# Kernel optimization log

Measured on AMD Instinct MI355X. Metric: run time of the kernel, lower is better.

## Reference

```python
import jax, jax.numpy as jnp
import numpy as np

B, S, D = 4, 2048, 1024
H = 16
HS = D // H  # 64


def setup_inputs() -> dict:
    key = jax.random.key(0)
    ks = jax.random.split(key, 6)
    scale = 1.0 / np.sqrt(D)
    x = jax.random.normal(ks[0], (B, S, D), dtype=jnp.float32)
    # per-head projection weights, stacked: [H, D, HS]
    Wq = jax.random.normal(ks[1], (H, D, HS), dtype=jnp.float32) * scale
    Wk = jax.random.normal(ks[2], (H, D, HS), dtype=jnp.float32) * scale
    Wv = jax.random.normal(ks[3], (H, D, HS), dtype=jnp.float32) * scale
    Wo = jax.random.normal(ks[4], (D, D), dtype=jnp.float32) * scale
    bo = jax.random.normal(ks[5], (D,), dtype=jnp.float32) * 0.01
    return {"x": x, "Wq": Wq, "Wk": Wk, "Wv": Wv, "Wo": Wo, "bo": bo}


def reference(x, Wq, Wk, Wv, Wo, bo):
    # Per-head dense projections (no bias): [B,S,D] x [H,D,HS] -> [B,H,S,HS]
    q = jnp.einsum('bsd,hde->bhse', x, Wq)
    k = jnp.einsum('bsd,hde->bhse', x, Wk)
    v = jnp.einsum('bsd,hde->bhse', x, Wv)
    # scaled dot-product scores: [B,H,S,S]
    scores = jnp.einsum('bhse,bhte->bhst', q, k) / jnp.sqrt(jnp.asarray(HS, dtype=x.dtype))
    # causal mask (lower triangular kept)
    causal = jnp.tril(jnp.ones((S, S), dtype=bool))
    scores = jnp.where(causal, scores, -jnp.inf)
    attn = jax.nn.softmax(scores, axis=-1)
    # dropout is identity at inference (rate handled as 0)
    out = jnp.einsum('bhst,bhte->bhse', attn, v)  # [B,H,S,HS]
    # concat heads: [B,S,H*HS] = [B,S,D]
    out = jnp.transpose(out, (0, 2, 1, 3)).reshape(B, S, D)
    return out @ Wo + bo
```

## Files before the change

kernel.cpp:

```cpp
#include <hip/hip_runtime.h>
#include <hip/hip_bf16.h>
#include <stdint.h>

#define NB 4
#define NS 2048
#define ND 1024
#define NH 16
#define NHS 64
#define NEG_BIG (-1e30f)
#define Q_SCALE 0.18033688011112042f

typedef __bf16 bf16x8 __attribute__((ext_vector_type(8)));
typedef float floatx4 __attribute__((ext_vector_type(4)));
typedef short s16x4 __attribute__((ext_vector_type(4)));

#if defined(__has_builtin)
#if __has_builtin(__builtin_amdgcn_mfma_f32_16x16x16bf16_1k)
#define HAVE_MFMA1K 1
#endif
#endif
#ifndef HAVE_MFMA1K
#define HAVE_MFMA1K 0
#endif

static constexpr size_t WSLAB = (size_t)NH * ND * NHS;
static constexpr size_t QSLAB = (size_t)NB * NH * NS * NHS;
static constexpr size_t XSLAB = (size_t)NB * NS * ND;

__device__ __forceinline__ uint16_t f2b(float f) {
    union { __hip_bfloat16 h; uint16_t u; } cv;
    cv.h = __float2bfloat16(f);
    return cv.u;
}

__device__ __forceinline__ void gll16(const void* g, void* l) {
  __builtin_amdgcn_global_load_lds(
      (__attribute__((address_space(1))) void*)(uintptr_t)g,
      (__attribute__((address_space(3))) void*)(uintptr_t)l,
      16, 0, 0);
}

__global__ __launch_bounds__(256) void k_prep(
    const float* __restrict__ x, const float* __restrict__ Wq,
    const float* __restrict__ Wk, const float* __restrict__ Wv,
    const float* __restrict__ Wo, uint16_t* __restrict__ xb,
    uint16_t* __restrict__ wt) {
  __shared__ __align__(16) uint16_t T[64][72];
  int bid = blockIdx.x;
  int tid = threadIdx.x;
  if (bid < 4096) {
    size_t i0 = ((size_t)bid * 256 + tid) * 8;
    float4 f0 = *(const float4*)&x[i0];
    float4 f1 = *(const float4*)&x[i0 + 4];
    __align__(16) uint16_t tmp[8];
    tmp[0] = f2b(f0.x); tmp[1] = f2b(f0.y); tmp[2] = f2b(f0.z); tmp[3] = f2b(f0.w);
    tmp[4] = f2b(f1.x); tmp[5] = f2b(f1.y); tmp[6] = f2b(f1.z); tmp[7] = f2b(f1.w);
    *(uint4*)&xb[i0] = *(uint4*)tmp;
    return;
  }
  bid -= 4096;
  const float* src; uint16_t* dst;
  int srcStride, dstStride, r0, c0;
  if (bid < 768) {
    int mat = bid >> 8;
    int rem = bid & 255;
    int h = rem >> 4, dt = rem & 15;
    const float* W = (mat == 0) ? Wq : (mat == 1) ? Wk : Wv;
    src = W + (size_t)h * (ND * NHS);
    dst = wt + (size_t)mat * WSLAB + (size_t)h * (NHS * ND);
    srcStride = NHS; dstStride = ND;
    r0 = dt * 64; c0 = 0;
  } else {
    int rem = bid - 768;
    int dt = rem >> 4, et = rem & 15;
    src = Wo; dst = wt + 3 * WSLAB;
    srcStride = ND; dstStride = ND;
    r0 = dt * 64; c0 = et * 64;
  }
  for (int u = tid; u < 1024; u += 256) {
    int row = u >> 4, cq = u & 15;
    float4 f = *(const float4*)&src[(size_t)(r0 + row) * srcStride + c0 + cq * 4];
    uint16_t* p = &T[row][cq * 4];
    p[0] = f2b(f.x); p[1] = f2b(f.y); p[2] = f2b(f.z); p[3] = f2b(f.w);
  }
  __syncthreads();
  for (int u = tid; u < 512; u += 256) {
    int c = u >> 3, cg = u & 7;
    __align__(16) uint16_t tmp[8];
    for (int j = 0; j < 8; j++) tmp[j] = T[cg * 8 + j][c];
    *(uint4*)&dst[(size_t)(c0 + c) * dstStride + r0 + cg * 8] = *(uint4*)tmp;
  }
}

__global__ __launch_bounds__(512, 4) void k_qkv(
    const uint16_t* __restrict__ xb, const uint16_t* __restrict__ wt,
    uint16_t* __restrict__ qk, uint16_t* __restrict__ vt) {
  __shared__ __align__(16) uint16_t L[32768];

  int bid = blockIdx.x;
  int xcd = bid & 7, idx = bid >> 3;
  int mtile = xcd * 8 + (idx & 7);
  int ntile = idx >> 3;
  int m0 = mtile * 128;
  int n0 = ntile * 128;

  int tid = threadIdx.x;
  int wave = tid >> 6, lane = tid & 63, quad = lane >> 4, l16 = lane & 15;
  int wr = wave >> 2, wc = wave & 3;

  int swc = ((tid & 3) ^ ((tid >> 4) & 3)) * 8;
  const uint16_t* pA = xb + (size_t)(m0 + (tid >> 2)) * ND + swc;
  const uint16_t* pB = wt + (size_t)(n0 + (tid >> 2)) * ND + swc;
  const int stOff = wave * 512;

  const int rq = (quad ^ (l16 >> 2)) * 8;
  const int offA = (wr * 64 + l16) * 32 + rq;
  const int offB = (wc * 32 + l16) * 32 + rq;

  floatx4 acc[4][2];
  #pragma unroll
  for (int i = 0; i < 4; i++)
    #pragma unroll
    for (int j = 0; j < 2; j++) acc[i][j] = (floatx4){0.f, 0.f, 0.f, 0.f};

#define STAGE(A_)                                                               \
  do {                                                                          \
    int a_ = (A_);                                                              \
    if (a_ < 32) {                                                              \
      int ko_ = (a_ >> 1) * 64 + (a_ & 1) * 32;                                 \
      gll16(pA + ko_, &L[(a_ & 3) * 4096 + stOff]);                             \
      gll16(pB + ko_, &L[16384 + (a_ & 3) * 4096 + stOff]);                     \
    }                                                                           \
  } while (0)

#define PH_BAR()                         \
  do {                                   \
    asm volatile("" ::: "memory");       \
    __builtin_amdgcn_s_barrier();        \
    asm volatile("" ::: "memory");       \
  } while (0)

  STAGE(0); STAGE(1); STAGE(2);
  asm volatile("s_waitcnt vmcnt(4)" ::: "memory");
  PH_BAR();

#define MFMA8()                                                                           \
  _Pragma("unroll")                                                                       \
  for (int mt_ = 0; mt_ < 4; mt_++)                                                       \
    _Pragma("unroll")                                                                     \
    for (int nt_ = 0; nt_ < 2; nt_++)                                                     \
      acc[mt_][nt_] = __builtin_amdgcn_mfma_f32_16x16x32_bf16(af[mt_], bfr[nt_], acc[mt_][nt_], 0, 0, 0)

  for (int t = 0; t < 16; ++t) {
    {
      int sA = ((2 * t) & 3) * 4096;
      int sB = 16384 + ((2 * t) & 3) * 4096;
      bf16x8 af[4], bfr[2];
      #pragma unroll
      for (int i = 0; i < 4; i++) af[i] = *(const bf16x8*)&L[sA + offA + i * 512];
      #pragma unroll
      for (int i = 0; i < 2; i++) bfr[i] = *(const bf16x8*)&L[sB + offB + i * 512];
      STAGE(2 * t + 3);
      PH_BAR();
      __builtin_amdgcn_s_setprio(1);
      MFMA8();
      __builtin_amdgcn_s_setprio(0);
      if (t < 15) { asm volatile("s_waitcnt vmcnt(4)" ::: "memory"); }
      else        { asm volatile("s_waitcnt vmcnt(0)" ::: "memory"); }
      PH_BAR();
    }
    {
      int sA = ((2 * t + 1) & 3) * 4096;
      int sB = 16384 + ((2 * t + 1) & 3) * 4096;
      bf16x8 af[4], bfr[2];
      #pragma unroll
      for (int i = 0; i < 4; i++) af[i] = *(const bf16x8*)&L[sA + offA + i * 512];
      #pragma unroll
      for (int i = 0; i < 2; i++) bfr[i] = *(const bf16x8*)&L[sB + offB + i * 512];
      STAGE(2 * t + 4);
      PH_BAR();
      __builtin_amdgcn_s_setprio(1);
      MFMA8();
      __builtin_amdgcn_s_setprio(0);
      if (t < 14)       { asm volatile("s_waitcnt vmcnt(4)" ::: "memory"); }
      else if (t == 14) { asm volatile("s_waitcnt vmcnt(2)" ::: "memory"); }
      if (t < 15) PH_BAR();
    }
  }
#undef MFMA8
#undef STAGE
#undef PH_BAR

  int matid = n0 >> 10;
  int b = m0 >> 11;
  if (matid == 2) {
    int hh = ((n0 - 2048) >> 6) + (wc >> 1);
    #pragma unroll
    for (int nt = 0; nt < 2; nt++) {
      int e = (wc & 1) * 32 + nt * 16 + l16;
      uint16_t* vrow = vt + ((size_t)(b * 16 + hh) * 64 + e) * NS;
      #pragma unroll
      for (int mt = 0; mt < 4; mt++) {
        __align__(8) uint16_t t4v[4];
        #pragma unroll
        for (int r = 0; r < 4; r++) t4v[r] = f2b(acc[mt][nt][r]);
        int s = (m0 & 2047) + wr * 64 + mt * 16 + quad * 4;
        *(uint2*)&vrow[s] = *(uint2*)t4v;
      }
    }
  } else {
    float scale = (matid == 0) ? Q_SCALE : 1.0f;
    uint16_t* base = qk + (size_t)matid * QSLAB;
    int hh = ((n0 & 1023) >> 6) + (wc >> 1);
    #pragma unroll
    for (int mt = 0; mt < 4; mt++) {
      int s = (m0 & 2047) + wr * 64 + mt * 16 + quad * 4;
      size_t rbase = ((size_t)(b * 16 + hh) * NS + s) * NHS;
      #pragma unroll
      for (int nt = 0; nt < 2; nt++)
        #pragma unroll
        for (int r = 0; r < 4; r++)
          base[rbase + (size_t)r * NHS + (wc & 1) * 32 + nt * 16 + l16] =
              f2b(acc[mt][nt][r] * scale);
    }
  }
}

#if HAVE_MFMA1K
__global__ __launch_bounds__(256, 4) void k_attn(
    const uint16_t* __restrict__ Q, const uint16_t* __restrict__ K,
    const uint16_t* __restrict__ VT, uint16_t* __restrict__ Y) {
  __shared__ __align__(16) uint16_t Ks[2][4096];
  __shared__ __align__(16) uint16_t Vs[2][4096];
  int bid = blockIdx.x;
  int bh = bid & 63;
  int w = bid >> 6;
  int ta = (w & 8) ? (15 - (w & 7)) : w;
  int b = bh >> 4, h = bh & 15;
  int tb = 31 - ta;
  const uint16_t* Qp = Q + (size_t)bh * (NS * NHS);
  const uint16_t* Kp = K + (size_t)bh * (NS * NHS);
  const uint16_t* Vp = VT + (size_t)bh * (NS * NHS);
  int tid = threadIdx.x;
  int wv = tid >> 6, lane = tid & 63, quad = lane >> 4, l16 = lane & 15;

  int srow = lane >> 3;
  int swOff = ((lane & 7) ^ srow) * 8;
  int stRow0 = wv * 16 + srow;
  int stRow1 = wv * 16 + 8 + srow;
  const int dst0 = wv * 1024;
  const int dst1 = wv * 1024 + 512;

#define STAGE_KV(KT, BUF)                                                         \
  do {                                                                            \
    int kt_ = (KT);                                                               \
    gll16(Kp + (size_t)(kt_ * 64 + stRow0) * NHS + swOff, &Ks[BUF][dst0]);        \
    gll16(Kp + (size_t)(kt_ * 64 + stRow1) * NHS + swOff, &Ks[BUF][dst1]);        \
    gll16(Vp + (size_t)stRow0 * NS + kt_ * 64 + swOff, &Vs[BUF][dst0]);           \
    gll16(Vp + (size_t)stRow1 * NS + kt_ * 64 + swOff, &Vs[BUF][dst1]);           \
  } while (0)

  int e3 = l16 & 7;
  int kc0 = (quad ^ e3) * 8;
  int kc1 = ((4 | quad) ^ e3) * 8;
  int vql = (quad & 1) * 4;
  int vqh = quad >> 1;
  int vcol[4];
  #pragma unroll
  for (int ct = 0; ct < 4; ct++)
    vcol[ct] = (((ct * 2 + vqh) ^ e3) * 8) + vql;

  int rA = ta * 64 + wv * 16 + l16;
  int rB = tb * 64 + wv * 16 + l16;
  bf16x8 aqA0 = *(const bf16x8*)&Qp[(size_t)rA * NHS + quad * 8];
  bf16x8 aqA1 = *(const bf16x8*)&Qp[(size_t)rA * NHS + 32 + quad * 8];
  bf16x8 aqB0 = *(const bf16x8*)&Qp[(size_t)rB * NHS + quad * 8];
  bf16x8 aqB1 = *(const bf16x8*)&Qp[(size_t)rB * NHS + 32 + quad * 8];

  float lAs = 0.f, lBs = 0.f;
  floatx4 oA[4], oB[4];
  for (int et = 0; et < 4; et++) {
    oA[et] = (floatx4){0.f, 0.f, 0.f, 0.f};
    oB[et] = (floatx4){0.f, 0.f, 0.f, 0.f};
  }

  STAGE_KV(0, 0);
  __syncthreads();

  for (int kt = 0; kt <= tb; kt++) {
    int cur = kt & 1;
    if (kt < tb) STAGE_KV(kt + 1, cur ^ 1);
    const uint16_t* KB = &Ks[cur][0];
    const uint16_t* VB = &Vs[cur][0];
    bool doA = (kt <= ta);

    s16x4 pbA[4], pbB[4];
    #pragma unroll
    for (int ct = 0; ct < 4; ct++) {
      int krow = (ct * 16 + l16) * 64;
      bf16x8 kb0 = *(const bf16x8*)&KB[krow + kc0];
      bf16x8 kb1 = *(const bf16x8*)&KB[krow + kc1];
      int key = kt * 64 + ct * 16 + quad * 4;
      floatx4 c = (floatx4){0.f, 0.f, 0.f, 0.f};
      c = __builtin_amdgcn_mfma_f32_16x16x32_bf16(kb0, aqB0, c, 0, 0, 0);
      c = __builtin_amdgcn_mfma_f32_16x16x32_bf16(kb1, aqB1, c, 0, 0, 0);
      #pragma unroll
      for (int r = 0; r < 4; r++) {
        float s = (kt == tb && key + r > rB) ? NEG_BIG : c[r];
        float p = __builtin_amdgcn_exp2f(s);
        lBs += p;
        pbB[ct][r] = (short)f2b(p);
      }
      if (doA) {
        floatx4 d = (floatx4){0.f, 0.f, 0.f, 0.f};
        d = __builtin_amdgcn_mfma_f32_16x16x32_bf16(kb0, aqA0, d, 0, 0, 0);
        d = __builtin_amdgcn_mfma_f32_16x16x32_bf16(kb1, aqA1, d, 0, 0, 0);
        #pragma unroll
        for (int r = 0; r < 4; r++) {
          float s = (kt == ta && key + r > rA) ? NEG_BIG : d[r];
          float p = __builtin_amdgcn_exp2f(s);
          lAs += p;
          pbA[ct][r] = (short)f2b(p);
        }
      }
    }
    #pragma unroll
    for (int et = 0; et < 4; et++) {
      int vrow = (et * 16 + l16) * 64;
      #pragma unroll
      for (int ct = 0; ct < 4; ct++) {
        s16x4 va = *(const s16x4*)&VB[vrow + vcol[ct]];
        oB[et] = __builtin_amdgcn_mfma_f32_16x16x16bf16_1k(va, pbB[ct], oB[et], 0, 0, 0);
        if (doA)
          oA[et] = __builtin_amdgcn_mfma_f32_16x16x16bf16_1k(va, pbA[ct], oA[et], 0, 0, 0);
      }
    }
    __syncthreads();
  }
#undef STAGE_KV

  lAs += __shfl_xor(lAs, 16, 64); lAs += __shfl_xor(lAs, 32, 64);
  lBs += __shfl_xor(lBs, 16, 64); lBs += __shfl_xor(lBs, 32, 64);
  float invA = 1.f / lAs, invB = 1.f / lBs;
  uint16_t* yb = Y + (size_t)b * NS * ND + (size_t)h * NHS;
  for (int et = 0; et < 4; et++) {
    __align__(8) uint16_t tA[4], tB[4];
    for (int r = 0; r < 4; r++) {
      tA[r] = f2b(oA[et][r] * invA);
      tB[r] = f2b(oB[et][r] * invB);
    }
    *(uint2*)&yb[(size_t)rA * ND + et * 16 + quad * 4] = *(uint2*)tA;
    *(uint2*)&yb[(size_t)rB * ND + et * 16 + quad * 4] = *(uint2*)tB;
  }
}
#else
__global__ __launch_bounds__(256) void k_attn(
    const uint16_t* __restrict__ Q, const uint16_t* __restrict__ K,
    const uint16_t* __restrict__ VT, uint16_t* __restrict__ Y) {
  __shared__ __align__(16) uint16_t Ks[64][72];
  __shared__ __align__(16) uint16_t Vs[64][72];
  __shared__ __align__(16) uint16_t Ps[4][2][16][72];
  int bid = blockIdx.x;
  int bh = bid & 63;
  int w = bid >> 6;
  int ta = (w & 8) ? (15 - (w & 7)) : w;
  int b = bh >> 4, h = bh & 15;
  int tb = 31 - ta;
  const uint16_t* Qp = Q + (size_t)bh * (NS * NHS);
  const uint16_t* Kp = K + (size_t)bh * (NS * NHS);
  const uint16_t* Vp = VT + (size_t)bh * (NS * NHS);
  int tid = threadIdx.x;
  int wv = tid >> 6, lane = tid & 63, quad = lane >> 4, l16 = lane & 15;

  int rA = ta * 64 + wv * 16 + l16;
  int rB = tb * 64 + wv * 16 + l16;
  bf16x8 aqA0 = *(const bf16x8*)&Qp[(size_t)rA * NHS + quad * 8];
  bf16x8 aqA1 = *(const bf16x8*)&Qp[(size_t)rA * NHS + 32 + quad * 8];
  bf16x8 aqB0 = *(const bf16x8*)&Qp[(size_t)rB * NHS + quad * 8];
  bf16x8 aqB1 = *(const bf16x8*)&Qp[(size_t)rB * NHS + 32 + quad * 8];

  float lA[4] = {0.f, 0.f, 0.f, 0.f}, lB[4] = {0.f, 0.f, 0.f, 0.f};
  floatx4 oA[4], oB[4];
  for (int ct = 0; ct < 4; ct++) {
    oA[ct] = (floatx4){0.f, 0.f, 0.f, 0.f};
    oB[ct] = (floatx4){0.f, 0.f, 0.f, 0.f};
  }
  for (int kt = 0; kt <= tb; kt++) {
    bool doA = (kt <= ta);
    __syncthreads();
    for (int u = tid; u < 512; u += 256) {
      int row = u >> 3, cg = u & 7;
      *(uint4*)&Ks[row][cg * 8] =
          *(const uint4*)&Kp[(size_t)(kt * 64 + row) * NHS + cg * 8];
    }
    for (int u = tid; u < 512; u += 256) {
      int row = u >> 3, cg = u & 7;
      *(uint4*)&Vs[row][cg * 8] =
          *(const uint4*)&Vp[(size_t)row * NS + kt * 64 + cg * 8];
    }
    __syncthreads();
    floatx4 sA[4], sB[4];
    for (int ct = 0; ct < 4; ct++) {
      bf16x8 kb0 = *(const bf16x8*)&Ks[ct * 16 + l16][quad * 8];
      bf16x8 kb1 = *(const bf16x8*)&Ks[ct * 16 + l16][32 + quad * 8];
      floatx4 c = (floatx4){0.f, 0.f, 0.f, 0.f};
      c = __builtin_amdgcn_mfma_f32_16x16x32_bf16(aqB0, kb0, c, 0, 0, 0);
      c = __builtin_amdgcn_mfma_f32_16x16x32_bf16(aqB1, kb1, c, 0, 0, 0);
      sB[ct] = c;
      if (doA) {
        floatx4 d = (floatx4){0.f, 0.f, 0.f, 0.f};
        d = __builtin_amdgcn_mfma_f32_16x16x32_bf16(aqA0, kb0, d, 0, 0, 0);
        d = __builtin_amdgcn_mfma_f32_16x16x32_bf16(aqA1, kb1, d, 0, 0, 0);
        sA[ct] = d;
      }
    }
    if (kt == tb) {
      int qrb = tb * 64 + wv * 16 + quad * 4;
      for (int ct = 0; ct < 4; ct++) {
        int kg = kt * 64 + ct * 16 + l16;
        for (int r = 0; r < 4; r++)
          sB[ct][r] = (kg <= qrb + r) ? sB[ct][r] : NEG_BIG;
      }
    }
    if (doA && kt == ta) {
      int qrb = ta * 64 + wv * 16 + quad * 4;
      for (int ct = 0; ct < 4; ct++) {
        int kg = kt * 64 + ct * 16 + l16;
        for (int r = 0; r < 4; r++)
          sA[ct][r] = (kg <= qrb + r) ? sA[ct][r] : NEG_BIG;
      }
    }
    for (int ct = 0; ct < 4; ct++)
      for (int r = 0; r < 4; r++) {
        float p = __builtin_amdgcn_exp2f(sB[ct][r]);
        lB[r] += p;
        Ps[wv][1][quad * 4 + r][ct * 16 + l16] = f2b(p);
      }
    if (doA)
      for (int ct = 0; ct < 4; ct++)
        for (int r = 0; r < 4; r++) {
          float p = __builtin_amdgcn_exp2f(sA[ct][r]);
          lA[r] += p;
          Ps[wv][0][quad * 4 + r][ct * 16 + l16] = f2b(p);
        }
    bf16x8 apB0 = *(const bf16x8*)&Ps[wv][1][l16][quad * 8];
    bf16x8 apB1 = *(const bf16x8*)&Ps[wv][1][l16][32 + quad * 8];
    bf16x8 apA0, apA1;
    if (doA) {
      apA0 = *(const bf16x8*)&Ps[wv][0][l16][quad * 8];
      apA1 = *(const bf16x8*)&Ps[wv][0][l16][32 + quad * 8];
    }
    for (int ct = 0; ct < 4; ct++) {
      bf16x8 vb0 = *(const bf16x8*)&Vs[ct * 16 + l16][quad * 8];
      bf16x8 vb1 = *(const bf16x8*)&Vs[ct * 16 + l16][32 + quad * 8];
      oB[ct] = __builtin_amdgcn_mfma_f32_16x16x32_bf16(apB0, vb0, oB[ct], 0, 0, 0);
      oB[ct] = __builtin_amdgcn_mfma_f32_16x16x32_bf16(apB1, vb1, oB[ct], 0, 0, 0);
      if (doA) {
        oA[ct] = __builtin_amdgcn_mfma_f32_16x16x32_bf16(apA0, vb0, oA[ct], 0, 0, 0);
        oA[ct] = __builtin_amdgcn_mfma_f32_16x16x32_bf16(apA1, vb1, oA[ct], 0, 0, 0);
      }
    }
  }
  for (int off = 1; off < 16; off <<= 1)
    for (int r = 0; r < 4; r++) {
      lA[r] += __shfl_xor(lA[r], off, 64);
      lB[r] += __shfl_xor(lB[r], off, 64);
    }
  uint16_t* yb = Y + (size_t)b * NS * ND + (size_t)h * NHS;
  for (int ct = 0; ct < 4; ct++)
    for (int r = 0; r < 4; r++) {
      int sA_ = ta * 64 + wv * 16 + quad * 4 + r;
      int sB_ = tb * 64 + wv * 16 + quad * 4 + r;
      yb[(size_t)sA_ * ND + ct * 16 + l16] = f2b(oA[ct][r] / lA[r]);
      yb[(size_t)sB_ * ND + ct * 16 + l16] = f2b(oB[ct][r] / lB[r]);
    }
}
#endif

__global__ __launch_bounds__(512, 4) void k_proj(
    const uint16_t* __restrict__ y, const uint16_t* __restrict__ wot,
    const float* __restrict__ bo, float* __restrict__ out) {
  __shared__ __align__(16) uint16_t L[32768];

  int bid = blockIdx.x;
  int xcd = bid & 7, idx = bid >> 3;
  int mtile = xcd * 8 + (idx & 7);
  int ntile = idx >> 3;
  int m0 = mtile * 128;
  int n0 = ntile * 128;

  int tid = threadIdx.x;
  int wave = tid >> 6, lane = tid & 63, quad = lane >> 4, l16 = lane & 15;
  int wr = wave >> 2, wc = wave & 3;

  int swc = ((tid & 3) ^ ((tid >> 4) & 3)) * 8;
  const uint16_t* pA = y + (size_t)(m0 + (tid >> 2)) * ND + swc;
  const uint16_t* pB = wot + (size_t)(n0 + (tid >> 2)) * ND + swc;
  const int stOff = wave * 512;

  const int rq = (quad ^ (l16 >> 2)) * 8;
  const int offA = (wr * 64 + l16) * 32 + rq;
  const int offB = (wc * 32 + l16) * 32 + rq;

  floatx4 acc[4][2];
  #pragma unroll
  for (int i = 0; i < 4; i++)
    #pragma unroll
    for (int j = 0; j < 2; j++) acc[i][j] = (floatx4){0.f, 0.f, 0.f, 0.f};

#define STAGE(A_)                                                               \
  do {                                                                          \
    int a_ = (A_);                                                              \
    if (a_ < 32) {                                                              \
      int ko_ = (a_ >> 1) * 64 + (a_ & 1) * 32;                                 \
      gll16(pA + ko_, &L[(a_ & 3) * 4096 + stOff]);                             \
      gll16(pB + ko_, &L[16384 + (a_ & 3) * 4096 + stOff]);                     \
    }                                                                           \
  } while (0)

#define PH_BAR()                         \
  do {                                   \
    asm volatile("" ::: "memory");       \
    __builtin_amdgcn_s_barrier();        \
    asm volatile("" ::: "memory");       \
  } while (0)

  STAGE(0); STAGE(1); STAGE(2);
  asm volatile("s_waitcnt vmcnt(4)" ::: "memory");
  PH_BAR();

#define MFMA8()                                                                           \
  _Pragma("unroll")                                                                       \
  for (int mt_ = 0; mt_ < 4; mt_++)                                                       \
    _Pragma("unroll")                                                                     \
    for (int nt_ = 0; nt_ < 2; nt_++)                                                     \
      acc[mt_][nt_] = __builtin_amdgcn_mfma_f32_16x16x32_bf16(af[mt_], bfr[nt_], acc[mt_][nt_], 0, 0, 0)

  for (int t = 0; t < 16; ++t) {
    {
      int sA = ((2 * t) & 3) * 4096;
      int sB = 16384 + ((2 * t) & 3) * 4096;
      bf16x8 af[4], bfr[2];
      #pragma unroll
      for (int i = 0; i < 4; i++) af[i] = *(const bf16x8*)&L[sA + offA + i * 512];
      #pragma unroll
      for (int i = 0; i < 2; i++) bfr[i] = *(const bf16x8*)&L[sB + offB + i * 512];
      STAGE(2 * t + 3);
      PH_BAR();
      __builtin_amdgcn_s_setprio(1);
      MFMA8();
      __builtin_amdgcn_s_setprio(0);
      if (t < 15) { asm volatile("s_waitcnt vmcnt(4)" ::: "memory"); }
      else        { asm volatile("s_waitcnt vmcnt(0)" ::: "memory"); }
      PH_BAR();
    }
    {
      int sA = ((2 * t + 1) & 3) * 4096;
      int sB = 16384 + ((2 * t + 1) & 3) * 4096;
      bf16x8 af[4], bfr[2];
      #pragma unroll
      for (int i = 0; i < 4; i++) af[i] = *(const bf16x8*)&L[sA + offA + i * 512];
      #pragma unroll
      for (int i = 0; i < 2; i++) bfr[i] = *(const bf16x8*)&L[sB + offB + i * 512];
      STAGE(2 * t + 4);
      PH_BAR();
      __builtin_amdgcn_s_setprio(1);
      MFMA8();
      __builtin_amdgcn_s_setprio(0);
      if (t < 14)       { asm volatile("s_waitcnt vmcnt(4)" ::: "memory"); }
      else if (t == 14) { asm volatile("s_waitcnt vmcnt(2)" ::: "memory"); }
      if (t < 15) PH_BAR();
    }
  }
#undef MFMA8
#undef STAGE
#undef PH_BAR

  float bv[2];
  #pragma unroll
  for (int nt = 0; nt < 2; nt++) bv[nt] = bo[n0 + wc * 32 + nt * 16 + l16];
  #pragma unroll
  for (int mt = 0; mt < 4; mt++) {
    int s = m0 + wr * 64 + mt * 16 + quad * 4;
    #pragma unroll
    for (int nt = 0; nt < 2; nt++) {
      int n = n0 + wc * 32 + nt * 16 + l16;
      #pragma unroll
      for (int r = 0; r < 4; r++)
        out[(size_t)(s + r) * ND + n] = acc[mt][nt][r] + bv[nt];
    }
  }
}

extern "C" void kernel_launch(void* const* d_in, const int* in_sizes, int n_in,
                              void* d_out, int out_size, void* d_ws, size_t ws_size,
                              hipStream_t stream) {
  const float* x  = (const float*)d_in[0];
  const float* Wq = (const float*)d_in[1];
  const float* Wk = (const float*)d_in[2];
  const float* Wv = (const float*)d_in[3];
  const float* Wo = (const float*)d_in[4];
  const float* bo = (const float*)d_in[5];
  uint16_t* ws = (uint16_t*)d_ws;

  uint16_t* wt = ws;
  uint16_t* xb = ws + 4 * WSLAB;
  uint16_t* q  = xb + XSLAB;
  uint16_t* k  = q + QSLAB;
  uint16_t* vt = k + QSLAB;
  uint16_t* y  = vt + QSLAB;

  k_prep<<<dim3(5120), dim3(256), 0, stream>>>(x, Wq, Wk, Wv, Wo, xb, wt);
  k_qkv<<<dim3(1536), dim3(512), 0, stream>>>(xb, wt, q, vt);
  k_attn<<<dim3(1024), dim3(256), 0, stream>>>(q, k, vt, y);
  k_proj<<<dim3(512), dim3(512), 0, stream>>>(y, wt + 3 * WSLAB, bo, (float*)d_out);
}
```

Baseline: 239.2 us.

## Switch GEMM K-loop to 64-wide double-buffered stages with syncthreads

Both the QKV and output-projection GEMM kernels replace the four-deep 32-wide K ring buffer, which used fine-grained vmcnt waits and two barriers per half-step, with a two-deep 64-wide stage buffer and one __syncthreads per 64-wide K step. The LDS swizzle changes to an 8-chunk XOR pattern over 64-element rows to match. The aim is fewer barriers and simpler bookkeeping per K step. In exchange, prefetch depth drops to one stage, and __syncthreads waits on all outstanding loads, so less global-load latency can be hidden behind the MFMAs.

```diff
diff --git a/kernel.cpp b/kernel.cpp
--- a/kernel.cpp
+++ b/kernel.cpp
@@ -108,14 +108,16 @@
   int wave = tid >> 6, lane = tid & 63, quad = lane >> 4, l16 = lane & 15;
   int wr = wave >> 2, wc = wave & 3;
 
-  int swc = ((tid & 3) ^ ((tid >> 4) & 3)) * 8;
-  const uint16_t* pA = xb + (size_t)(m0 + (tid >> 2)) * ND + swc;
-  const uint16_t* pB = wt + (size_t)(n0 + (tid >> 2)) * ND + swc;
+  int swc = ((tid & 7) ^ ((tid >> 3) & 7)) * 8;
+  const uint16_t* pA = xb + (size_t)(m0 + (tid >> 3)) * ND + swc;
+  const uint16_t* pB = wt + (size_t)(n0 + (tid >> 3)) * ND + swc;
   const int stOff = wave * 512;
 
-  const int rq = (quad ^ (l16 >> 2)) * 8;
-  const int offA = (wr * 64 + l16) * 32 + rq;
-  const int offB = (wc * 32 + l16) * 32 + rq;
+  int e3 = l16 & 7;
+  const int rowA = (wr * 64 + l16) * 64;
+  const int rowB = 8192 + (wc * 32 + l16) * 64;
+  const int ck0 = (quad ^ e3) * 8;
+  const int ck1 = ((4 | quad) ^ e3) * 8;
 
   floatx4 acc[4][2];
   #pragma unroll
@@ -123,26 +125,15 @@
     #pragma unroll
     for (int j = 0; j < 2; j++) acc[i][j] = (floatx4){0.f, 0.f, 0.f, 0.f};
 
-#define STAGE(A_)                                                               \
+#define STAGE_T(T, BUF)                                                         \
   do {                                                                          \
-    int a_ = (A_);                                                              \
-    if (a_ < 32) {                                                              \
-      int ko_ = (a_ >> 1) * 64 + (a_ & 1) * 32;                                 \
-      gll16(pA + ko_, &L[(a_ & 3) * 4096 + stOff]);                             \
-      gll16(pB + ko_, &L[16384 + (a_ & 3) * 4096 + stOff]);                     \
-    }                                                                           \
+    int kb_ = (T) * 64;                                                         \
+    int lb_ = (BUF) * 16384;                                                    \
+    gll16(pA + kb_, &L[lb_ + stOff]);                                           \
+    gll16(pA + 64 * ND + kb_, &L[lb_ + 4096 + stOff]);                          \
+    gll16(pB + kb_, &L[lb_ + 8192 + stOff]);                                    \
+    gll16(pB + 64 * ND + kb_, &L[lb_ + 12288 + stOff]);                         \
   } while (0)
-
-#define PH_BAR()                         \
-  do {                                   \
-    asm volatile("" ::: "memory");       \
-    __builtin_amdgcn_s_barrier();        \
-    asm volatile("" ::: "memory");       \
-  } while (0)
-
-  STAGE(0); STAGE(1); STAGE(2);
-  asm volatile("s_waitcnt vmcnt(4)" ::: "memory");
-  PH_BAR();
 
 #define MFMA8()                                                                           \
   _Pragma("unroll")                                                                       \
@@ -151,45 +142,37 @@
     for (int nt_ = 0; nt_ < 2; nt_++)                                                     \
       acc[mt_][nt_] = __builtin_amdgcn_mfma_f32_16x16x32_bf16(af[mt_], bfr[nt_], acc[mt_][nt_], 0, 0, 0)
 
+  STAGE_T(0, 0);
+  __syncthreads();
+
   for (int t = 0; t < 16; ++t) {
+    int cur = t & 1;
+    if (t < 15) STAGE_T(t + 1, cur ^ 1);
+    const int base = cur * 16384;
     {
-      int sA = ((2 * t) & 3) * 4096;
-      int sB = 16384 + ((2 * t) & 3) * 4096;
       bf16x8 af[4], bfr[2];
       #pragma unroll
-      for (int i = 0; i < 4; i++) af[i] = *(const bf16x8*)&L[sA + offA + i * 512];
-      #pragma unroll
-      for (int i = 0; i < 2; i++) bfr[i] = *(const bf16x8*)&L[sB + offB + i * 512];
-      STAGE(2 * t + 3);
-      PH_BAR();
+      for (int i = 0; i < 4; i++) af[i] = *(const bf16x8*)&L[base + rowA + i * 1024 + ck0];
+      #pragma unroll
+      for (int j = 0; j < 2; j++) bfr[j] = *(const bf16x8*)&L[base + rowB + j * 1024 + ck0];
       __builtin_amdgcn_s_setprio(1);
       MFMA8();
       __builtin_amdgcn_s_setprio(0);
-      if (t < 15) { asm volatile("s_waitcnt vmcnt(4)" ::: "memory"); }
-      else        { asm volatile("s_waitcnt vmcnt(0)" ::: "memory"); }
-      PH_BAR();
     }
     {
-      int sA = ((2 * t + 1) & 3) * 4096;
-      int sB = 16384 + ((2 * t + 1) & 3) * 4096;
       bf16x8 af[4], bfr[2];
       #pragma unroll
-      for (int i = 0; i < 4; i++) af[i] = *(const bf16x8*)&L[sA + offA + i * 512];
-      #pragma unroll
-      for (int i = 0; i < 2; i++) bfr[i] = *(const bf16x8*)&L[sB + offB + i * 512];
-      STAGE(2 * t + 4);
-      PH_BAR();
+      for (int i = 0; i < 4; i++) af[i] = *(const bf16x8*)&L[base + rowA + i * 1024 + ck1];
+      #pragma unroll
+      for (int j = 0; j < 2; j++) bfr[j] = *(const bf16x8*)&L[base + rowB + j * 1024 + ck1];
       __builtin_amdgcn_s_setprio(1);
       MFMA8();
       __builtin_amdgcn_s_setprio(0);
-      if (t < 14)       { asm volatile("s_waitcnt vmcnt(4)" ::: "memory"); }
-      else if (t == 14) { asm volatile("s_waitcnt vmcnt(2)" ::: "memory"); }
-      if (t < 15) PH_BAR();
-    }
+    }
+    if (t < 15) __syncthreads();
   }
 #undef MFMA8
-#undef STAGE
-#undef PH_BAR
+#undef STAGE_T
 
   int matid = n0 >> 10;
   int b = m0 >> 11;
@@ -493,14 +476,16 @@
   int wave = tid >> 6, lane = tid & 63, quad = lane >> 4, l16 = lane & 15;
   int wr = wave >> 2, wc = wave & 3;
 
-  int swc = ((tid & 3) ^ ((tid >> 4) & 3)) * 8;
-  const uint16_t* pA = y + (size_t)(m0 + (tid >> 2)) * ND + swc;
-  const uint16_t* pB = wot + (size_t)(n0 + (tid >> 2)) * ND + swc;
+  int swc = ((tid & 7) ^ ((tid >> 3) & 7)) * 8;
+  const uint16_t* pA = y + (size_t)(m0 + (tid >> 3)) * ND + swc;
+  const uint16_t* pB = wot + (size_t)(n0 + (tid >> 3)) * ND + swc;
   const int stOff = wave * 512;
 
-  const int rq = (quad ^ (l16 >> 2)) * 8;
-  const int offA = (wr * 64 + l16) * 32 + rq;
-  const int offB = (wc * 32 + l16) * 32 + rq;
+  int e3 = l16 & 7;
+  const int rowA = (wr * 64 + l16) * 64;
+  const int rowB = 8192 + (wc * 32 + l16) * 64;
+  const int ck0 = (quad ^ e3) * 8;
+  const int ck1 = ((4 | quad) ^ e3) * 8;
 
   floatx4 acc[4][2];
   #pragma unroll
@@ -508,26 +493,15 @@
     #pragma unroll
     for (int j = 0; j < 2; j++) acc[i][j] = (floatx4){0.f, 0.f, 0.f, 0.f};
 
-#define STAGE(A_)                                                               \
+#define STAGE_T(T, BUF)                                                         \
   do {                                                                          \
-    int a_ = (A_);                                                              \
-    if (a_ < 32) {                                                              \
-      int ko_ = (a_ >> 1) * 64 + (a_ & 1) * 32;                                 \
-      gll16(pA + ko_, &L[(a_ & 3) * 4096 + stOff]);                             \
-      gll16(pB + ko_, &L[16384 + (a_ & 3) * 4096 + stOff]);                     \
-    }                                                                           \
+    int kb_ = (T) * 64;                                                         \
+    int lb_ = (BUF) * 16384;                                                    \
+    gll16(pA + kb_, &L[lb_ + stOff]);                                           \
+    gll16(pA + 64 * ND + kb_, &L[lb_ + 4096 + stOff]);                          \
+    gll16(pB + kb_, &L[lb_ + 8192 + stOff]);                                    \
+    gll16(pB + 64 * ND + kb_, &L[lb_ + 12288 + stOff]);                         \
   } while (0)
-
-#define PH_BAR()                         \
-  do {                                   \
-    asm volatile("" ::: "memory");       \
-    __builtin_amdgcn_s_barrier();        \
-    asm volatile("" ::: "memory");       \
-  } while (0)
-
-  STAGE(0); STAGE(1); STAGE(2);
-  asm volatile("s_waitcnt vmcnt(4)" ::: "memory");
-  PH_BAR();
 
 #define MFMA8()                                                                           \
   _Pragma("unroll")                                                                       \
@@ -536,45 +510,37 @@
     for (int nt_ = 0; nt_ < 2; nt_++)                                                     \
       acc[mt_][nt_] = __builtin_amdgcn_mfma_f32_16x16x32_bf16(af[mt_], bfr[nt_], acc[mt_][nt_], 0, 0, 0)
 
+  STAGE_T(0, 0);
+  __syncthreads();
+
   for (int t = 0; t < 16; ++t) {
+    int cur = t & 1;
+    if (t < 15) STAGE_T(t + 1, cur ^ 1);
+    const int base = cur * 16384;
     {
-      int sA = ((2 * t) & 3) * 4096;
-      int sB = 16384 + ((2 * t) & 3) * 4096;
       bf16x8 af[4], bfr[2];
       #pragma unroll
-      for (int i = 0; i < 4; i++) af[i] = *(const bf16x8*)&L[sA + offA + i * 512];
-      #pragma unroll
-      for (int i = 0; i < 2; i++) bfr[i] = *(const bf16x8*)&L[sB + offB + i * 512];
-      STAGE(2 * t + 3);
-      PH_BAR();
+      for (int i = 0; i < 4; i++) af[i] = *(const bf16x8*)&L[base + rowA + i * 1024 + ck0];
+      #pragma unroll
+      for (int j = 0; j < 2; j++) bfr[j] = *(const bf16x8*)&L[base + rowB + j * 1024 + ck0];
       __builtin_amdgcn_s_setprio(1);
       MFMA8();
       __builtin_amdgcn_s_setprio(0);
-      if (t < 15) { asm volatile("s_waitcnt vmcnt(4)" ::: "memory"); }
-      else        { asm volatile("s_waitcnt vmcnt(0)" ::: "memory"); }
-      PH_BAR();
     }
     {
-      int sA = ((2 * t + 1) & 3) * 4096;
-      int sB = 16384 + ((2 * t + 1) & 3) * 4096;
       bf16x8 af[4], bfr[2];
       #pragma unroll
-      for (int i = 0; i < 4; i++) af[i] = *(const bf16x8*)&L[sA + offA + i * 512];
-      #pragma unroll
-      for (int i = 0; i < 2; i++) bfr[i] = *(const bf16x8*)&L[sB + offB + i * 512];
-      STAGE(2 * t + 4);
-      PH_BAR();
+      for (int i = 0; i < 4; i++) af[i] = *(const bf16x8*)&L[base + rowA + i * 1024 + ck1];
+      #pragma unroll
+      for (int j = 0; j < 2; j++) bfr[j] = *(const bf16x8*)&L[base + rowB + j * 1024 + ck1];
       __builtin_amdgcn_s_setprio(1);
       MFMA8();
       __builtin_amdgcn_s_setprio(0);
-      if (t < 14)       { asm volatile("s_waitcnt vmcnt(4)" ::: "memory"); }
-      else if (t == 14) { asm volatile("s_waitcnt vmcnt(2)" ::: "memory"); }
-      if (t < 15) PH_BAR();
-    }
+    }
+    if (t < 15) __syncthreads();
   }
 #undef MFMA8
-#undef STAGE
-#undef PH_BAR
+#undef STAGE_T
 
   float bv[2];
   #pragma unroll
```

After: 228.8 us. 1.05x faster.
